# Kernel tuning notes

Measured on AMD Instinct MI355X. Metric: run time of the kernel, lower is better.

Reference implementation:

```python
import jax, jax.numpy as jnp
import numpy as np

NUM_NODES = 50000
NUM_HYPEREDGES = 20000
NNZ = 1600000
IN_DIM = 256
OUT_DIM = 128


def setup_inputs() -> dict:
    key = jax.random.key(0)
    k1, k2, k3, k4, k5 = jax.random.split(key, 5)
    x = jax.random.normal(k1, (NUM_NODES, IN_DIM), dtype=jnp.float32)
    node_idx = jax.random.randint(k2, (NNZ,), 0, NUM_NODES)
    edge_idx = jax.random.randint(k3, (NNZ,), 0, NUM_HYPEREDGES)
    hyperedge_index = jnp.stack([node_idx, edge_idx], axis=0)  # [2, nnz]
    # glorot-style init for HypergraphConv's internal Linear (bias=False)
    scale = np.sqrt(6.0 / (IN_DIM + OUT_DIM)).astype(np.float32)
    lin_weight = jax.random.uniform(k4, (IN_DIM, OUT_DIM), dtype=jnp.float32,
                                    minval=-scale, maxval=scale)
    bias = jnp.zeros((OUT_DIM,), dtype=jnp.float32)
    return {"x_node_features": x, "lin_weight": lin_weight, "bias": bias,
            "hyperedge_index": hyperedge_index}


def reference(x_node_features, lin_weight, bias, hyperedge_index):
    src = hyperedge_index[0]   # node ids   [nnz]
    edge = hyperedge_index[1]  # hyperedge ids [nnz]
    ones = jnp.ones_like(src, dtype=x_node_features.dtype)

    # X Theta
    xw = x_node_features @ lin_weight  # [N, F_out]

    # D^{-1}: node degree (hyperedge weights default to 1)
    deg_n = jax.ops.segment_sum(ones, src, num_segments=NUM_NODES)
    d_inv = jnp.where(deg_n > 0, 1.0 / deg_n, 0.0)
    # B^{-1}: hyperedge cardinality
    deg_e = jax.ops.segment_sum(ones, edge, num_segments=NUM_HYPEREDGES)
    b_inv = jnp.where(deg_e > 0, 1.0 / deg_e, 0.0)

    # node -> hyperedge: m_e = B_e^{-1} * sum_{i in e} (X Theta)_i
    m_e = jax.ops.segment_sum(xw[src], edge, num_segments=NUM_HYPEREDGES)
    m_e = m_e * b_inv[:, None]  # [E, F_out]

    # hyperedge -> node: out_i = D_i^{-1} * sum_{e ni i} m_e
    out = jax.ops.segment_sum(m_e[edge], src, num_segments=NUM_NODES)
    out = out * d_inv[:, None] + bias  # [N, F_out]

    # ReLU + mean pool over nodes
    return jnp.mean(jax.nn.relu(out), axis=0)  # [F_out]
```

## Files before the change

kernel.cpp:

```cpp
#include <hip/hip_runtime.h>

#define NUM_N 50000
#define NUM_E 20000
#define IN_DIM 256
#define OUT_DIM 128
#define NBE 1250
#define NBN 1563
#define ECAP 1536
#define NCAP 1280
#define SCAT_CHUNK 4096
#define NGEMM 782
#define XSCALE 16.0f

typedef unsigned short ushort_t;
typedef unsigned int uint_t;

__device__ __forceinline__ int clamp8(int q) { return min(max(q, -127), 127); }
__device__ __forceinline__ int lo8(uint_t u) { return (int)(signed char)(u & 0xff); }
__device__ __forceinline__ int hi8(uint_t u) { return ((int)(short)(ushort_t)u) >> 8; }

__global__ void init_kernel(int* __restrict__ gcur_e, int* __restrict__ gcur_n,
                            float* __restrict__ macc) {
    int t = blockIdx.x * 1024 + threadIdx.x;
    if (t < NBE) gcur_e[t] = t * ECAP;
    if (t < NBN) gcur_n[t] = t * NCAP;
    if (t < 128) macc[t] = 0.f;
}

__global__ __launch_bounds__(256) void gemm_scatter_kernel(
        const float* __restrict__ x, const float* __restrict__ w,
        char* __restrict__ xw, int nrows,
        const int* __restrict__ node_idx, const int* __restrict__ edge_idx, int nnz,
        int* __restrict__ gcur_e, int* __restrict__ gcur_n,
        uint_t* __restrict__ stag_e, uint_t* __restrict__ stag_n) {
    __shared__ int smem[6208];
    int tid = threadIdx.x;

    if (blockIdx.x >= NGEMM) {
        int* lh    = smem;
        int* lbase = smem + 2813;
        int bid = blockIdx.x - NGEMM;
        int nblk = gridDim.x - NGEMM;
        for (int cbase = bid * SCAT_CHUNK; cbase < nnz; cbase += nblk * SCAT_CHUNK) {
            int cend = min(cbase + SCAT_CHUNK, nnz);
            for (int i = tid; i < NBE + NBN; i += 256) lh[i] = 0;
            __syncthreads();
            for (int i = cbase + tid; i < cend; i += 256) {
                atomicAdd(&lh[edge_idx[i] >> 4], 1);
                atomicAdd(&lh[NBE + (node_idx[i] >> 5)], 1);
            }
            __syncthreads();
            for (int i = tid; i < NBE; i += 256) {
                int c = lh[i];
                lbase[i] = c ? atomicAdd(&gcur_e[i], c) : 0;
            }
            for (int i = tid; i < NBN; i += 256) {
                int c = lh[NBE + i];
                lbase[NBE + i] = c ? atomicAdd(&gcur_n[i], c) : 0;
            }
            __syncthreads();
            for (int i = tid; i < NBE + NBN; i += 256) lh[i] = 0;
            __syncthreads();
            for (int i = cbase + tid; i < cend; i += 256) {
                int v = node_idx[i];
                int e = edge_idx[i];
                uint_t pk = ((uint_t)v << 16) | (uint_t)e;
                int be = e >> 4;
                int bn = NBE + (v >> 5);
                int pe = lbase[be] + atomicAdd(&lh[be], 1);
                if (pe < (be + 1) * ECAP) stag_e[pe] = pk;
                int pn = lbase[bn] + atomicAdd(&lh[bn], 1);
                if (pn < (bn - NBE + 1) * NCAP) stag_n[pn] = pk;
            }
            __syncthreads();
        }
        return;
    }

    float* As = (float*)smem;
    float* Ws = (float*)smem + 2112;
    int block_row = blockIdx.x * 64;
    int rg = tid >> 4;
    int cg = tid & 15;
    int r0 = rg * 4, c0 = cg * 8;
    float acc[4][8] = {};
    for (int k0 = 0; k0 < IN_DIM; k0 += 32) {
#pragma unroll
        for (int rep = 0; rep < 2; ++rep) {
            int f = tid + rep * 256;
            int row = f >> 3, kq = f & 7;
            float4 v = make_float4(0.f, 0.f, 0.f, 0.f);
            int grow = block_row + row;
            if (grow < nrows) v = *(const float4*)&x[(size_t)grow * IN_DIM + k0 + kq * 4];
            As[row * 33 + kq * 4 + 0] = v.x;
            As[row * 33 + kq * 4 + 1] = v.y;
            As[row * 33 + kq * 4 + 2] = v.z;
            As[row * 33 + kq * 4 + 3] = v.w;
        }
#pragma unroll
        for (int rep = 0; rep < 4; ++rep) {
            int f = tid + rep * 256;
            int kk = f >> 5, cq = f & 31;
            float4 v = *(const float4*)&w[(size_t)(k0 + kk) * OUT_DIM + cq * 4];
            *(float4*)&Ws[kk * 128 + cq * 4] = v;
        }
        __syncthreads();
#pragma unroll
        for (int k = 0; k < 32; ++k) {
            float av[4];
#pragma unroll
            for (int i = 0; i < 4; ++i) av[i] = As[(r0 + i) * 33 + k];
            float4 b0 = *(const float4*)&Ws[k * 128 + c0];
            float4 b1 = *(const float4*)&Ws[k * 128 + c0 + 4];
            float bv[8] = {b0.x, b0.y, b0.z, b0.w, b1.x, b1.y, b1.z, b1.w};
#pragma unroll
            for (int i = 0; i < 4; ++i)
#pragma unroll
                for (int j = 0; j < 8; ++j)
                    acc[i][j] += av[i] * bv[j];
        }
        __syncthreads();
    }
#pragma unroll
    for (int i = 0; i < 4; ++i) {
        int grow = block_row + r0 + i;
        if (grow < nrows) {
            int q[8];
#pragma unroll
            for (int j = 0; j < 8; ++j) q[j] = clamp8(__float2int_rn(acc[i][j] * XSCALE));
            uint2 pk;
            pk.x = (uint_t)(q[0] & 0xff) | ((uint_t)(q[1] & 0xff) << 8) |
                   ((uint_t)(q[2] & 0xff) << 16) | ((uint_t)(q[3] & 0xff) << 24);
            pk.y = (uint_t)(q[4] & 0xff) | ((uint_t)(q[5] & 0xff) << 8) |
                   ((uint_t)(q[6] & 0xff) << 16) | ((uint_t)(q[7] & 0xff) << 24);
            *(uint2*)&xw[(size_t)grow * OUT_DIM + c0] = pk;
        }
    }
}

__global__ __launch_bounds__(256) void edge_agg_kernel(const uint_t* __restrict__ stag_e,
                                                       const int* __restrict__ gcur_e,
                                                       const ushort_t* __restrict__ xw16,
                                                       ushort_t* __restrict__ me16) {
    __shared__ int acc[16 * 128];
    __shared__ int cnt[16];
    int tid = threadIdx.x;
    int lane = tid & 63;
    int wid = tid >> 6;
    int b = blockIdx.x;
    for (int i = tid; i < 16 * 128; i += 256) acc[i] = 0;
    if (tid < 16) cnt[tid] = 0;
    __syncthreads();
    int beg = b * ECAP, end = gcur_e[b];
    int cb = beg + wid * 8;
    for (; cb + 8 <= end; cb += 32) {
        uint4 pa = *(const uint4*)&stag_e[cb];
        uint4 pb = *(const uint4*)&stag_e[cb + 4];
        uint_t u0 = xw16[(size_t)(pa.x >> 16) * 64 + lane];
        uint_t u1 = xw16[(size_t)(pa.y >> 16) * 64 + lane];
        uint_t u2 = xw16[(size_t)(pa.z >> 16) * 64 + lane];
        uint_t u3 = xw16[(size_t)(pa.w >> 16) * 64 + lane];
        uint_t u4 = xw16[(size_t)(pb.x >> 16) * 64 + lane];
        uint_t u5 = xw16[(size_t)(pb.y >> 16) * 64 + lane];
        uint_t u6 = xw16[(size_t)(pb.z >> 16) * 64 + lane];
        uint_t u7 = xw16[(size_t)(pb.w >> 16) * 64 + lane];
        int r0 = (pa.x & 15) * 128, r1 = (pa.y & 15) * 128;
        int r2 = (pa.z & 15) * 128, r3 = (pa.w & 15) * 128;
        int r4 = (pb.x & 15) * 128, r5 = (pb.y & 15) * 128;
        int r6 = (pb.z & 15) * 128, r7 = (pb.w & 15) * 128;
        atomicAdd(&acc[r0 + lane],      lo8(u0));
        atomicAdd(&acc[r0 + 64 + lane], hi8(u0));
        atomicAdd(&acc[r1 + lane],      lo8(u1));
        atomicAdd(&acc[r1 + 64 + lane], hi8(u1));
        atomicAdd(&acc[r2 + lane],      lo8(u2));
        atomicAdd(&acc[r2 + 64 + lane], hi8(u2));
        atomicAdd(&acc[r3 + lane],      lo8(u3));
        atomicAdd(&acc[r3 + 64 + lane], hi8(u3));
        atomicAdd(&acc[r4 + lane],      lo8(u4));
        atomicAdd(&acc[r4 + 64 + lane], hi8(u4));
        atomicAdd(&acc[r5 + lane],      lo8(u5));
        atomicAdd(&acc[r5 + 64 + lane], hi8(u5));
        atomicAdd(&acc[r6 + lane],      lo8(u6));
        atomicAdd(&acc[r6 + 64 + lane], hi8(u6));
        atomicAdd(&acc[r7 + lane],      lo8(u7));
        atomicAdd(&acc[r7 + 64 + lane], hi8(u7));
        if (lane == 0) {
            atomicAdd(&cnt[pa.x & 15], 1);
            atomicAdd(&cnt[pa.y & 15], 1);
            atomicAdd(&cnt[pa.z & 15], 1);
            atomicAdd(&cnt[pa.w & 15], 1);
            atomicAdd(&cnt[pb.x & 15], 1);
            atomicAdd(&cnt[pb.y & 15], 1);
            atomicAdd(&cnt[pb.z & 15], 1);
            atomicAdd(&cnt[pb.w & 15], 1);
        }
    }
    if (cb < end) {
        uint4 pa = *(const uint4*)&stag_e[cb];
        uint4 pb = *(const uint4*)&stag_e[cb + 4];
        int m = end - cb;
        bool w1 = m > 1, w2 = m > 2, w3 = m > 3, w4 = m > 4, w5 = m > 5, w6 = m > 6;
        uint_t u0 = xw16[(size_t)(pa.x >> 16) * 64 + lane];
        uint_t u1 = xw16[(size_t)(pa.y >> 16) * 64 + lane];
        uint_t u2 = xw16[(size_t)(pa.z >> 16) * 64 + lane];
        uint_t u3 = xw16[(size_t)(pa.w >> 16) * 64 + lane];
        uint_t u4 = xw16[(size_t)(pb.x >> 16) * 64 + lane];
        uint_t u5 = xw16[(size_t)(pb.y >> 16) * 64 + lane];
        uint_t u6 = xw16[(size_t)(pb.z >> 16) * 64 + lane];
        int r0 = (pa.x & 15) * 128, r1 = (pa.y & 15) * 128;
        int r2 = (pa.z & 15) * 128, r3 = (pa.w & 15) * 128;
        int r4 = (pb.x & 15) * 128, r5 = (pb.y & 15) * 128, r6 = (pb.z & 15) * 128;
        atomicAdd(&acc[r0 + lane],      lo8(u0));
        atomicAdd(&acc[r0 + 64 + lane], hi8(u0));
        atomicAdd(&acc[r1 + lane],      w1 ? lo8(u1) : 0);
        atomicAdd(&acc[r1 + 64 + lane], w1 ? hi8(u1) : 0);
        atomicAdd(&acc[r2 + lane],      w2 ? lo8(u2) : 0);
        atomicAdd(&acc[r2 + 64 + lane], w2 ? hi8(u2) : 0);
        atomicAdd(&acc[r3 + lane],      w3 ? lo8(u3) : 0);
        atomicAdd(&acc[r3 + 64 + lane], w3 ? hi8(u3) : 0);
        atomicAdd(&acc[r4 + lane],      w4 ? lo8(u4) : 0);
        atomicAdd(&acc[r4 + 64 + lane], w4 ? hi8(u4) : 0);
        atomicAdd(&acc[r5 + lane],      w5 ? lo8(u5) : 0);
        atomicAdd(&acc[r5 + 64 + lane], w5 ? hi8(u5) : 0);
        atomicAdd(&acc[r6 + lane],      w6 ? lo8(u6) : 0);
        atomicAdd(&acc[r6 + 64 + lane], w6 ? hi8(u6) : 0);
        if (lane == 0) {
            atomicAdd(&cnt[pa.x & 15], 1);
            if (w1) atomicAdd(&cnt[pa.y & 15], 1);
            if (w2) atomicAdd(&cnt[pa.z & 15], 1);
            if (w3) atomicAdd(&cnt[pa.w & 15], 1);
            if (w4) atomicAdd(&cnt[pb.x & 15], 1);
            if (w5) atomicAdd(&cnt[pb.y & 15], 1);
            if (w6) atomicAdd(&cnt[pb.z & 15], 1);
        }
    }
    __syncthreads();
    for (int r = wid; r < 16; r += 4) {
        int e = b * 16 + r;
        int c = cnt[r];
        float f = c ? 4.0f / (float)c : 0.f;
        int q0 = clamp8(__float2int_rn((float)acc[r * 128 + lane] * f));
        int q1 = clamp8(__float2int_rn((float)acc[r * 128 + 64 + lane] * f));
        me16[(size_t)e * 64 + lane] = (ushort_t)((q0 & 0xff) | ((q1 & 0xff) << 8));
    }
}

__global__ __launch_bounds__(256) void node_agg_kernel(const uint_t* __restrict__ stag_n,
                                                       const int* __restrict__ gcur_n,
                                                       const ushort_t* __restrict__ me16,
                                                       const float* __restrict__ bias,
                                                       float* __restrict__ mean_acc) {
    __shared__ int acc[32 * 128];
    __shared__ int cnt[32];
    int tid = threadIdx.x;
    int lane = tid & 63;
    int wid = tid >> 6;
    int b = blockIdx.x;
    for (int i = tid; i < 32 * 128; i += 256) acc[i] = 0;
    if (tid < 32) cnt[tid] = 0;
    __syncthreads();
    int beg = b * NCAP, end = gcur_n[b];
    int cb = beg + wid * 8;
    for (; cb + 8 <= end; cb += 32) {
        uint4 pa = *(const uint4*)&stag_n[cb];
        uint4 pb = *(const uint4*)&stag_n[cb + 4];
        uint_t u0 = me16[(size_t)(pa.x & 0xffff) * 64 + lane];
        uint_t u1 = me16[(size_t)(pa.y & 0xffff) * 64 + lane];
        uint_t u2 = me16[(size_t)(pa.z & 0xffff) * 64 + lane];
        uint_t u3 = me16[(size_t)(pa.w & 0xffff) * 64 + lane];
        uint_t u4 = me16[(size_t)(pb.x & 0xffff) * 64 + lane];
        uint_t u5 = me16[(size_t)(pb.y & 0xffff) * 64 + lane];
        uint_t u6 = me16[(size_t)(pb.z & 0xffff) * 64 + lane];
        uint_t u7 = me16[(size_t)(pb.w & 0xffff) * 64 + lane];
        int r0 = ((pa.x >> 16) & 31) * 128, r1 = ((pa.y >> 16) & 31) * 128;
        int r2 = ((pa.z >> 16) & 31) * 128, r3 = ((pa.w >> 16) & 31) * 128;
        int r4 = ((pb.x >> 16) & 31) * 128, r5 = ((pb.y >> 16) & 31) * 128;
        int r6 = ((pb.z >> 16) & 31) * 128, r7 = ((pb.w >> 16) & 31) * 128;
        atomicAdd(&acc[r0 + lane],      lo8(u0));
        atomicAdd(&acc[r0 + 64 + lane], hi8(u0));
        atomicAdd(&acc[r1 + lane],      lo8(u1));
        atomicAdd(&acc[r1 + 64 + lane], hi8(u1));
        atomicAdd(&acc[r2 + lane],      lo8(u2));
        atomicAdd(&acc[r2 + 64 + lane], hi8(u2));
        atomicAdd(&acc[r3 + lane],      lo8(u3));
        atomicAdd(&acc[r3 + 64 + lane], hi8(u3));
        atomicAdd(&acc[r4 + lane],      lo8(u4));
        atomicAdd(&acc[r4 + 64 + lane], hi8(u4));
        atomicAdd(&acc[r5 + lane],      lo8(u5));
        atomicAdd(&acc[r5 + 64 + lane], hi8(u5));
        atomicAdd(&acc[r6 + lane],      lo8(u6));
        atomicAdd(&acc[r6 + 64 + lane], hi8(u6));
        atomicAdd(&acc[r7 + lane],      lo8(u7));
        atomicAdd(&acc[r7 + 64 + lane], hi8(u7));
        if (lane == 0) {
            atomicAdd(&cnt[(pa.x >> 16) & 31], 1);
            atomicAdd(&cnt[(pa.y >> 16) & 31], 1);
            atomicAdd(&cnt[(pa.z >> 16) & 31], 1);
            atomicAdd(&cnt[(pa.w >> 16) & 31], 1);
            atomicAdd(&cnt[(pb.x >> 16) & 31], 1);
            atomicAdd(&cnt[(pb.y >> 16) & 31], 1);
            atomicAdd(&cnt[(pb.z >> 16) & 31], 1);
            atomicAdd(&cnt[(pb.w >> 16) & 31], 1);
        }
    }
    if (cb < end) {
        uint4 pa = *(const uint4*)&stag_n[cb];
        uint4 pb = *(const uint4*)&stag_n[cb + 4];
        int m = end - cb;
        bool w1 = m > 1, w2 = m > 2, w3 = m > 3, w4 = m > 4, w5 = m > 5, w6 = m > 6;
        uint_t u0 = me16[(size_t)(pa.x & 0xffff) * 64 + lane];
        uint_t u1 = me16[(size_t)(pa.y & 0xffff) * 64 + lane];
        uint_t u2 = me16[(size_t)(pa.z & 0xffff) * 64 + lane];
        uint_t u3 = me16[(size_t)(pa.w & 0xffff) * 64 + lane];
        uint_t u4 = me16[(size_t)(pb.x & 0xffff) * 64 + lane];
        uint_t u5 = me16[(size_t)(pb.y & 0xffff) * 64 + lane];
        uint_t u6 = me16[(size_t)(pb.z & 0xffff) * 64 + lane];
        int r0 = ((pa.x >> 16) & 31) * 128, r1 = ((pa.y >> 16) & 31) * 128;
        int r2 = ((pa.z >> 16) & 31) * 128, r3 = ((pa.w >> 16) & 31) * 128;
        int r4 = ((pb.x >> 16) & 31) * 128, r5 = ((pb.y >> 16) & 31) * 128;
        int r6 = ((pb.z >> 16) & 31) * 128;
        atomicAdd(&acc[r0 + lane],      lo8(u0));
        atomicAdd(&acc[r0 + 64 + lane], hi8(u0));
        atomicAdd(&acc[r1 + lane],      w1 ? lo8(u1) : 0);
        atomicAdd(&acc[r1 + 64 + lane], w1 ? hi8(u1) : 0);
        atomicAdd(&acc[r2 + lane],      w2 ? lo8(u2) : 0);
        atomicAdd(&acc[r2 + 64 + lane], w2 ? hi8(u2) : 0);
        atomicAdd(&acc[r3 + lane],      w3 ? lo8(u3) : 0);
        atomicAdd(&acc[r3 + 64 + lane], w3 ? hi8(u3) : 0);
        atomicAdd(&acc[r4 + lane],      w4 ? lo8(u4) : 0);
        atomicAdd(&acc[r4 + 64 + lane], w4 ? hi8(u4) : 0);
        atomicAdd(&acc[r5 + lane],      w5 ? lo8(u5) : 0);
        atomicAdd(&acc[r5 + 64 + lane], w5 ? hi8(u5) : 0);
        atomicAdd(&acc[r6 + lane],      w6 ? lo8(u6) : 0);
        atomicAdd(&acc[r6 + 64 + lane], w6 ? hi8(u6) : 0);
        if (lane == 0) {
            atomicAdd(&cnt[(pa.x >> 16) & 31], 1);
            if (w1) atomicAdd(&cnt[(pa.y >> 16) & 31], 1);
            if (w2) atomicAdd(&cnt[(pa.z >> 16) & 31], 1);
            if (w3) atomicAdd(&cnt[(pa.w >> 16) & 31], 1);
            if (w4) atomicAdd(&cnt[(pb.x >> 16) & 31], 1);
            if (w5) atomicAdd(&cnt[(pb.y >> 16) & 31], 1);
            if (w6) atomicAdd(&cnt[(pb.z >> 16) & 31], 1);
        }
    }
    __syncthreads();
    if (tid < 128) {
        int c = tid;
        int sw = (c & 1) ? (64 + (c >> 1)) : (c >> 1);
        float bc = bias[c];
        float s = 0.f;
        int nmax = min(32, NUM_N - b * 32);
        for (int r = 0; r < nmax; ++r) {
            int cc = cnt[r];
            float dinv = cc ? 1.0f / (64.0f * (float)cc) : 0.f;
            s += fmaxf((float)acc[r * 128 + sw] * dinv + bc, 0.f);
        }
        atomicAdd(&mean_acc[c], s);
    }
}

__global__ void finalize_kernel(const float* __restrict__ mean_acc, float* __restrict__ out) {
    int t = threadIdx.x;
    if (t < 128) out[t] = mean_acc[t] * (1.0f / (float)NUM_N);
}

extern "C" void kernel_launch(void* const* d_in, const int* in_sizes, int n_in,
                              void* d_out, int out_size, void* d_ws, size_t ws_size,
                              hipStream_t stream) {
    const float* x    = (const float*)d_in[0];
    const float* w    = (const float*)d_in[1];
    const float* bias = (const float*)d_in[2];
    const int*   hei  = (const int*)d_in[3];
    int nnz = in_sizes[3] / 2;
    const int* node_idx = hei;
    const int* edge_idx = hei + nnz;
    float* out = (float*)d_out;

    char* ws = (char*)d_ws;
    char*     xw     = ws;
    ushort_t* me16   = (ushort_t*)(ws + 6400000);
    uint_t*   stag_e = (uint_t*)(ws + 8960000);
    uint_t*   stag_n = (uint_t*)(ws + 16640032);
    int* gcur_e = (int*)(ws + 24642624);
    int* gcur_n = (int*)(ws + 24647624);
    float* macc = (float*)(ws + 24653876);

    int nscat = (nnz + SCAT_CHUNK - 1) / SCAT_CHUNK;

    init_kernel<<<2, 1024, 0, stream>>>(gcur_e, gcur_n, macc);
    gemm_scatter_kernel<<<NGEMM + nscat, 256, 0, stream>>>(
        x, w, xw, NUM_N, node_idx, edge_idx, nnz, gcur_e, gcur_n, stag_e, stag_n);

    edge_agg_kernel<<<NBE, 256, 0, stream>>>(stag_e, gcur_e, (const ushort_t*)xw, me16);
    node_agg_kernel<<<NBN, 256, 0, stream>>>(stag_n, gcur_n, me16, bias, macc);
    finalize_kernel<<<1, 128, 0, stream>>>(macc, out);
}
```

Before: 220.9 us.

## Shard global bucket cursors into eight classes to reduce atomic contention

The scatter blocks now reserve space in one of eight per-class copies of each edge and node bucket, selected by block index, instead of a single shared cursor per bucket. The aggregation kernels then loop over all eight class sub-buckets for their bucket. The aim is to cut contention on the global atomicAdd cursors during the scatter phase. In exchange the workspace grows, there are more cursors to initialise, and the reads become fragmented into eight smaller ranges with more tail handling. The smaller per-class capacities also raise the chance that a sub-bucket overflows and entries are silently dropped.

```diff
diff --git a/kernel.cpp b/kernel.cpp
--- a/kernel.cpp
+++ b/kernel.cpp
@@ -6,8 +6,9 @@
 #define OUT_DIM 128
 #define NBE 1250
 #define NBN 1563
-#define ECAP 1536
-#define NCAP 1280
+#define NCLS 8
+#define ECAPC 256
+#define NCAPC 192
 #define SCAT_CHUNK 4096
 #define NGEMM 782
 #define XSCALE 16.0f
@@ -22,8 +23,8 @@
 __global__ void init_kernel(int* __restrict__ gcur_e, int* __restrict__ gcur_n,
                             float* __restrict__ macc) {
     int t = blockIdx.x * 1024 + threadIdx.x;
-    if (t < NBE) gcur_e[t] = t * ECAP;
-    if (t < NBN) gcur_n[t] = t * NCAP;
+    if (t < NCLS * NBE) gcur_e[t] = t * ECAPC;
+    if (t < NCLS * NBN) gcur_n[t] = t * NCAPC;
     if (t < 128) macc[t] = 0.f;
 }
 
@@ -39,6 +40,7 @@
     if (blockIdx.x >= NGEMM) {
         int* lh    = smem;
         int* lbase = smem + 2813;
+        int cls = blockIdx.x & (NCLS - 1);
         int bid = blockIdx.x - NGEMM;
         int nblk = gridDim.x - NGEMM;
         for (int cbase = bid * SCAT_CHUNK; cbase < nnz; cbase += nblk * SCAT_CHUNK) {
@@ -52,11 +54,11 @@
             __syncthreads();
             for (int i = tid; i < NBE; i += 256) {
                 int c = lh[i];
-                lbase[i] = c ? atomicAdd(&gcur_e[i], c) : 0;
+                lbase[i] = c ? atomicAdd(&gcur_e[cls * NBE + i], c) : 0;
             }
             for (int i = tid; i < NBN; i += 256) {
                 int c = lh[NBE + i];
-                lbase[NBE + i] = c ? atomicAdd(&gcur_n[i], c) : 0;
+                lbase[NBE + i] = c ? atomicAdd(&gcur_n[cls * NBN + i], c) : 0;
             }
             __syncthreads();
             for (int i = tid; i < NBE + NBN; i += 256) lh[i] = 0;
@@ -66,11 +68,11 @@
                 int e = edge_idx[i];
                 uint_t pk = ((uint_t)v << 16) | (uint_t)e;
                 int be = e >> 4;
-                int bn = NBE + (v >> 5);
+                int bn = v >> 5;
                 int pe = lbase[be] + atomicAdd(&lh[be], 1);
-                if (pe < (be + 1) * ECAP) stag_e[pe] = pk;
-                int pn = lbase[bn] + atomicAdd(&lh[bn], 1);
-                if (pn < (bn - NBE + 1) * NCAP) stag_n[pn] = pk;
+                if (pe < (cls * NBE + be + 1) * ECAPC) stag_e[pe] = pk;
+                int pn = lbase[NBE + bn] + atomicAdd(&lh[NBE + bn], 1);
+                if (pn < (cls * NBN + bn + 1) * NCAPC) stag_n[pn] = pk;
             }
             __syncthreads();
         }
@@ -151,87 +153,91 @@
     for (int i = tid; i < 16 * 128; i += 256) acc[i] = 0;
     if (tid < 16) cnt[tid] = 0;
     __syncthreads();
-    int beg = b * ECAP, end = gcur_e[b];
-    int cb = beg + wid * 8;
-    for (; cb + 8 <= end; cb += 32) {
-        uint4 pa = *(const uint4*)&stag_e[cb];
-        uint4 pb = *(const uint4*)&stag_e[cb + 4];
-        uint_t u0 = xw16[(size_t)(pa.x >> 16) * 64 + lane];
-        uint_t u1 = xw16[(size_t)(pa.y >> 16) * 64 + lane];
-        uint_t u2 = xw16[(size_t)(pa.z >> 16) * 64 + lane];
-        uint_t u3 = xw16[(size_t)(pa.w >> 16) * 64 + lane];
-        uint_t u4 = xw16[(size_t)(pb.x >> 16) * 64 + lane];
-        uint_t u5 = xw16[(size_t)(pb.y >> 16) * 64 + lane];
-        uint_t u6 = xw16[(size_t)(pb.z >> 16) * 64 + lane];
-        uint_t u7 = xw16[(size_t)(pb.w >> 16) * 64 + lane];
-        int r0 = (pa.x & 15) * 128, r1 = (pa.y & 15) * 128;
-        int r2 = (pa.z & 15) * 128, r3 = (pa.w & 15) * 128;
-        int r4 = (pb.x & 15) * 128, r5 = (pb.y & 15) * 128;
-        int r6 = (pb.z & 15) * 128, r7 = (pb.w & 15) * 128;
-        atomicAdd(&acc[r0 + lane],      lo8(u0));
-        atomicAdd(&acc[r0 + 64 + lane], hi8(u0));
-        atomicAdd(&acc[r1 + lane],      lo8(u1));
-        atomicAdd(&acc[r1 + 64 + lane], hi8(u1));
-        atomicAdd(&acc[r2 + lane],      lo8(u2));
-        atomicAdd(&acc[r2 + 64 + lane], hi8(u2));
-        atomicAdd(&acc[r3 + lane],      lo8(u3));
-        atomicAdd(&acc[r3 + 64 + lane], hi8(u3));
-        atomicAdd(&acc[r4 + lane],      lo8(u4));
-        atomicAdd(&acc[r4 + 64 + lane], hi8(u4));
-        atomicAdd(&acc[r5 + lane],      lo8(u5));
-        atomicAdd(&acc[r5 + 64 + lane], hi8(u5));
-        atomicAdd(&acc[r6 + lane],      lo8(u6));
-        atomicAdd(&acc[r6 + 64 + lane], hi8(u6));
-        atomicAdd(&acc[r7 + lane],      lo8(u7));
-        atomicAdd(&acc[r7 + 64 + lane], hi8(u7));
-        if (lane == 0) {
-            atomicAdd(&cnt[pa.x & 15], 1);
-            atomicAdd(&cnt[pa.y & 15], 1);
-            atomicAdd(&cnt[pa.z & 15], 1);
-            atomicAdd(&cnt[pa.w & 15], 1);
-            atomicAdd(&cnt[pb.x & 15], 1);
-            atomicAdd(&cnt[pb.y & 15], 1);
-            atomicAdd(&cnt[pb.z & 15], 1);
-            atomicAdd(&cnt[pb.w & 15], 1);
-        }
-    }
-    if (cb < end) {
-        uint4 pa = *(const uint4*)&stag_e[cb];
-        uint4 pb = *(const uint4*)&stag_e[cb + 4];
-        int m = end - cb;
-        bool w1 = m > 1, w2 = m > 2, w3 = m > 3, w4 = m > 4, w5 = m > 5, w6 = m > 6;
-        uint_t u0 = xw16[(size_t)(pa.x >> 16) * 64 + lane];
-        uint_t u1 = xw16[(size_t)(pa.y >> 16) * 64 + lane];
-        uint_t u2 = xw16[(size_t)(pa.z >> 16) * 64 + lane];
-        uint_t u3 = xw16[(size_t)(pa.w >> 16) * 64 + lane];
-        uint_t u4 = xw16[(size_t)(pb.x >> 16) * 64 + lane];
-        uint_t u5 = xw16[(size_t)(pb.y >> 16) * 64 + lane];
-        uint_t u6 = xw16[(size_t)(pb.z >> 16) * 64 + lane];
-        int r0 = (pa.x & 15) * 128, r1 = (pa.y & 15) * 128;
-        int r2 = (pa.z & 15) * 128, r3 = (pa.w & 15) * 128;
-        int r4 = (pb.x & 15) * 128, r5 = (pb.y & 15) * 128, r6 = (pb.z & 15) * 128;
-        atomicAdd(&acc[r0 + lane],      lo8(u0));
-        atomicAdd(&acc[r0 + 64 + lane], hi8(u0));
-        atomicAdd(&acc[r1 + lane],      w1 ? lo8(u1) : 0);
-        atomicAdd(&acc[r1 + 64 + lane], w1 ? hi8(u1) : 0);
-        atomicAdd(&acc[r2 + lane],      w2 ? lo8(u2) : 0);
-        atomicAdd(&acc[r2 + 64 + lane], w2 ? hi8(u2) : 0);
-        atomicAdd(&acc[r3 + lane],      w3 ? lo8(u3) : 0);
-        atomicAdd(&acc[r3 + 64 + lane], w3 ? hi8(u3) : 0);
-        atomicAdd(&acc[r4 + lane],      w4 ? lo8(u4) : 0);
-        atomicAdd(&acc[r4 + 64 + lane], w4 ? hi8(u4) : 0);
-        atomicAdd(&acc[r5 + lane],      w5 ? lo8(u5) : 0);
-        atomicAdd(&acc[r5 + 64 + lane], w5 ? hi8(u5) : 0);
-        atomicAdd(&acc[r6 + lane],      w6 ? lo8(u6) : 0);
-        atomicAdd(&acc[r6 + 64 + lane], w6 ? hi8(u6) : 0);
-        if (lane == 0) {
-            atomicAdd(&cnt[pa.x & 15], 1);
-            if (w1) atomicAdd(&cnt[pa.y & 15], 1);
-            if (w2) atomicAdd(&cnt[pa.z & 15], 1);
-            if (w3) atomicAdd(&cnt[pa.w & 15], 1);
-            if (w4) atomicAdd(&cnt[pb.x & 15], 1);
-            if (w5) atomicAdd(&cnt[pb.y & 15], 1);
-            if (w6) atomicAdd(&cnt[pb.z & 15], 1);
+    for (int cls = 0; cls < NCLS; ++cls) {
+        int idx = cls * NBE + b;
+        int beg = idx * ECAPC;
+        int end = min(gcur_e[idx], beg + ECAPC);
+        int cb = beg + wid * 8;
+        for (; cb + 8 <= end; cb += 32) {
+            uint4 pa = *(const uint4*)&stag_e[cb];
+            uint4 pb = *(const uint4*)&stag_e[cb + 4];
+            uint_t u0 = xw16[(size_t)(pa.x >> 16) * 64 + lane];
+            uint_t u1 = xw16[(size_t)(pa.y >> 16) * 64 + lane];
+            uint_t u2 = xw16[(size_t)(pa.z >> 16) * 64 + lane];
+            uint_t u3 = xw16[(size_t)(pa.w >> 16) * 64 + lane];
+            uint_t u4 = xw16[(size_t)(pb.x >> 16) * 64 + lane];
+            uint_t u5 = xw16[(size_t)(pb.y >> 16) * 64 + lane];
+            uint_t u6 = xw16[(size_t)(pb.z >> 16) * 64 + lane];
+            uint_t u7 = xw16[(size_t)(pb.w >> 16) * 64 + lane];
+            int r0 = (pa.x & 15) * 128, r1 = (pa.y & 15) * 128;
+            int r2 = (pa.z & 15) * 128, r3 = (pa.w & 15) * 128;
+            int r4 = (pb.x & 15) * 128, r5 = (pb.y & 15) * 128;
+            int r6 = (pb.z & 15) * 128, r7 = (pb.w & 15) * 128;
+            atomicAdd(&acc[r0 + lane],      lo8(u0));
+            atomicAdd(&acc[r0 + 64 + lane], hi8(u0));
+            atomicAdd(&acc[r1 + lane],      lo8(u1));
+            atomicAdd(&acc[r1 + 64 + lane], hi8(u1));
+            atomicAdd(&acc[r2 + lane],      lo8(u2));
+            atomicAdd(&acc[r2 + 64 + lane], hi8(u2));
+            atomicAdd(&acc[r3 + lane],      lo8(u3));
+            atomicAdd(&acc[r3 + 64 + lane], hi8(u3));
+            atomicAdd(&acc[r4 + lane],      lo8(u4));
+            atomicAdd(&acc[r4 + 64 + lane], hi8(u4));
+            atomicAdd(&acc[r5 + lane],      lo8(u5));
+            atomicAdd(&acc[r5 + 64 + lane], hi8(u5));
+            atomicAdd(&acc[r6 + lane],      lo8(u6));
+            atomicAdd(&acc[r6 + 64 + lane], hi8(u6));
+            atomicAdd(&acc[r7 + lane],      lo8(u7));
+            atomicAdd(&acc[r7 + 64 + lane], hi8(u7));
+            if (lane == 0) {
+                atomicAdd(&cnt[pa.x & 15], 1);
+                atomicAdd(&cnt[pa.y & 15], 1);
+                atomicAdd(&cnt[pa.z & 15], 1);
+                atomicAdd(&cnt[pa.w & 15], 1);
+                atomicAdd(&cnt[pb.x & 15], 1);
+                atomicAdd(&cnt[pb.y & 15], 1);
+                atomicAdd(&cnt[pb.z & 15], 1);
+                atomicAdd(&cnt[pb.w & 15], 1);
+            }
+        }
+        if (cb < end) {
+            uint4 pa = *(const uint4*)&stag_e[cb];
+            uint4 pb = *(const uint4*)&stag_e[cb + 4];
+            int m = end - cb;
+            bool w1 = m > 1, w2 = m > 2, w3 = m > 3, w4 = m > 4, w5 = m > 5, w6 = m > 6;
+            uint_t u0 = xw16[(size_t)(pa.x >> 16) * 64 + lane];
+            uint_t u1 = xw16[(size_t)(pa.y >> 16) * 64 + lane];
+            uint_t u2 = xw16[(size_t)(pa.z >> 16) * 64 + lane];
+            uint_t u3 = xw16[(size_t)(pa.w >> 16) * 64 + lane];
+            uint_t u4 = xw16[(size_t)(pb.x >> 16) * 64 + lane];
+            uint_t u5 = xw16[(size_t)(pb.y >> 16) * 64 + lane];
+            uint_t u6 = xw16[(size_t)(pb.z >> 16) * 64 + lane];
+            int r0 = (pa.x & 15) * 128, r1 = (pa.y & 15) * 128;
+            int r2 = (pa.z & 15) * 128, r3 = (pa.w & 15) * 128;
+            int r4 = (pb.x & 15) * 128, r5 = (pb.y & 15) * 128, r6 = (pb.z & 15) * 128;
+            atomicAdd(&acc[r0 + lane],      lo8(u0));
+            atomicAdd(&acc[r0 + 64 + lane], hi8(u0));
+            atomicAdd(&acc[r1 + lane],      w1 ? lo8(u1) : 0);
+            atomicAdd(&acc[r1 + 64 + lane], w1 ? hi8(u1) : 0);
+            atomicAdd(&acc[r2 + lane],      w2 ? lo8(u2) : 0);
+            atomicAdd(&acc[r2 + 64 + lane], w2 ? hi8(u2) : 0);
+            atomicAdd(&acc[r3 + lane],      w3 ? lo8(u3) : 0);
+            atomicAdd(&acc[r3 + 64 + lane], w3 ? hi8(u3) : 0);
+            atomicAdd(&acc[r4 + lane],      w4 ? lo8(u4) : 0);
+            atomicAdd(&acc[r4 + 64 + lane], w4 ? hi8(u4) : 0);
+            atomicAdd(&acc[r5 + lane],      w5 ? lo8(u5) : 0);
+            atomicAdd(&acc[r5 + 64 + lane], w5 ? hi8(u5) : 0);
+            atomicAdd(&acc[r6 + lane],      w6 ? lo8(u6) : 0);
+            atomicAdd(&acc[r6 + 64 + lane], w6 ? hi8(u6) : 0);
+            if (lane == 0) {
+                atomicAdd(&cnt[pa.x & 15], 1);
+                if (w1) atomicAdd(&cnt[pa.y & 15], 1);
+                if (w2) atomicAdd(&cnt[pa.z & 15], 1);
+                if (w3) atomicAdd(&cnt[pa.w & 15], 1);
+                if (w4) atomicAdd(&cnt[pb.x & 15], 1);
+                if (w5) atomicAdd(&cnt[pb.y & 15], 1);
+                if (w6) atomicAdd(&cnt[pb.z & 15], 1);
+            }
         }
     }
     __syncthreads();
@@ -259,88 +265,92 @@
     for (int i = tid; i < 32 * 128; i += 256) acc[i] = 0;
     if (tid < 32) cnt[tid] = 0;
     __syncthreads();
-    int beg = b * NCAP, end = gcur_n[b];
-    int cb = beg + wid * 8;
-    for (; cb + 8 <= end; cb += 32) {
-        uint4 pa = *(const uint4*)&stag_n[cb];
-        uint4 pb = *(const uint4*)&stag_n[cb + 4];
-        uint_t u0 = me16[(size_t)(pa.x & 0xffff) * 64 + lane];
-        uint_t u1 = me16[(size_t)(pa.y & 0xffff) * 64 + lane];
-        uint_t u2 = me16[(size_t)(pa.z & 0xffff) * 64 + lane];
-        uint_t u3 = me16[(size_t)(pa.w & 0xffff) * 64 + lane];
-        uint_t u4 = me16[(size_t)(pb.x & 0xffff) * 64 + lane];
-        uint_t u5 = me16[(size_t)(pb.y & 0xffff) * 64 + lane];
-        uint_t u6 = me16[(size_t)(pb.z & 0xffff) * 64 + lane];
-        uint_t u7 = me16[(size_t)(pb.w & 0xffff) * 64 + lane];
-        int r0 = ((pa.x >> 16) & 31) * 128, r1 = ((pa.y >> 16) & 31) * 128;
-        int r2 = ((pa.z >> 16) & 31) * 128, r3 = ((pa.w >> 16) & 31) * 128;
-        int r4 = ((pb.x >> 16) & 31) * 128, r5 = ((pb.y >> 16) & 31) * 128;
-        int r6 = ((pb.z >> 16) & 31) * 128, r7 = ((pb.w >> 16) & 31) * 128;
-        atomicAdd(&acc[r0 + lane],      lo8(u0));
-        atomicAdd(&acc[r0 + 64 + lane], hi8(u0));
-        atomicAdd(&acc[r1 + lane],      lo8(u1));
-        atomicAdd(&acc[r1 + 64 + lane], hi8(u1));
-        atomicAdd(&acc[r2 + lane],      lo8(u2));
-        atomicAdd(&acc[r2 + 64 + lane], hi8(u2));
-        atomicAdd(&acc[r3 + lane],      lo8(u3));
-        atomicAdd(&acc[r3 + 64 + lane], hi8(u3));
-        atomicAdd(&acc[r4 + lane],      lo8(u4));
-        atomicAdd(&acc[r4 + 64 + lane], hi8(u4));
-        atomicAdd(&acc[r5 + lane],      lo8(u5));
-        atomicAdd(&acc[r5 + 64 + lane], hi8(u5));
-        atomicAdd(&acc[r6 + lane],      lo8(u6));
-        atomicAdd(&acc[r6 + 64 + lane], hi8(u6));
-        atomicAdd(&acc[r7 + lane],      lo8(u7));
-        atomicAdd(&acc[r7 + 64 + lane], hi8(u7));
-        if (lane == 0) {
-            atomicAdd(&cnt[(pa.x >> 16) & 31], 1);
-            atomicAdd(&cnt[(pa.y >> 16) & 31], 1);
-            atomicAdd(&cnt[(pa.z >> 16) & 31], 1);
-            atomicAdd(&cnt[(pa.w >> 16) & 31], 1);
-            atomicAdd(&cnt[(pb.x >> 16) & 31], 1);
-            atomicAdd(&cnt[(pb.y >> 16) & 31], 1);
-            atomicAdd(&cnt[(pb.z >> 16) & 31], 1);
-            atomicAdd(&cnt[(pb.w >> 16) & 31], 1);
-        }
-    }
-    if (cb < end) {
-        uint4 pa = *(const uint4*)&stag_n[cb];
-        uint4 pb = *(const uint4*)&stag_n[cb + 4];
-        int m = end - cb;
-        bool w1 = m > 1, w2 = m > 2, w3 = m > 3, w4 = m > 4, w5 = m > 5, w6 = m > 6;
-        uint_t u0 = me16[(size_t)(pa.x & 0xffff) * 64 + lane];
-        uint_t u1 = me16[(size_t)(pa.y & 0xffff) * 64 + lane];
-        uint_t u2 = me16[(size_t)(pa.z & 0xffff) * 64 + lane];
-        uint_t u3 = me16[(size_t)(pa.w & 0xffff) * 64 + lane];
-        uint_t u4 = me16[(size_t)(pb.x & 0xffff) * 64 + lane];
-        uint_t u5 = me16[(size_t)(pb.y & 0xffff) * 64 + lane];
-        uint_t u6 = me16[(size_t)(pb.z & 0xffff) * 64 + lane];
-        int r0 = ((pa.x >> 16) & 31) * 128, r1 = ((pa.y >> 16) & 31) * 128;
-        int r2 = ((pa.z >> 16) & 31) * 128, r3 = ((pa.w >> 16) & 31) * 128;
-        int r4 = ((pb.x >> 16) & 31) * 128, r5 = ((pb.y >> 16) & 31) * 128;
-        int r6 = ((pb.z >> 16) & 31) * 128;
-        atomicAdd(&acc[r0 + lane],      lo8(u0));
-        atomicAdd(&acc[r0 + 64 + lane], hi8(u0));
-        atomicAdd(&acc[r1 + lane],      w1 ? lo8(u1) : 0);
-        atomicAdd(&acc[r1 + 64 + lane], w1 ? hi8(u1) : 0);
-        atomicAdd(&acc[r2 + lane],      w2 ? lo8(u2) : 0);
-        atomicAdd(&acc[r2 + 64 + lane], w2 ? hi8(u2) : 0);
-        atomicAdd(&acc[r3 + lane],      w3 ? lo8(u3) : 0);
-        atomicAdd(&acc[r3 + 64 + lane], w3 ? hi8(u3) : 0);
-        atomicAdd(&acc[r4 + lane],      w4 ? lo8(u4) : 0);
-        atomicAdd(&acc[r4 + 64 + lane], w4 ? hi8(u4) : 0);
-        atomicAdd(&acc[r5 + lane],      w5 ? lo8(u5) : 0);
-        atomicAdd(&acc[r5 + 64 + lane], w5 ? hi8(u5) : 0);
-        atomicAdd(&acc[r6 + lane],      w6 ? lo8(u6) : 0);
-        atomicAdd(&acc[r6 + 64 + lane], w6 ? hi8(u6) : 0);
-        if (lane == 0) {
-            atomicAdd(&cnt[(pa.x >> 16) & 31], 1);
-            if (w1) atomicAdd(&cnt[(pa.y >> 16) & 31], 1);
-            if (w2) atomicAdd(&cnt[(pa.z >> 16) & 31], 1);
-            if (w3) atomicAdd(&cnt[(pa.w >> 16) & 31], 1);
-            if (w4) atomicAdd(&cnt[(pb.x >> 16) & 31], 1);
-            if (w5) atomicAdd(&cnt[(pb.y >> 16) & 31], 1);
-            if (w6) atomicAdd(&cnt[(pb.z >> 16) & 31], 1);
+    for (int cls = 0; cls < NCLS; ++cls) {
+        int idx = cls * NBN + b;
+        int beg = idx * NCAPC;
+        int end = min(gcur_n[idx], beg + NCAPC);
+        int cb = beg + wid * 8;
+        for (; cb + 8 <= end; cb += 32) {
+            uint4 pa = *(const uint4*)&stag_n[cb];
+            uint4 pb = *(const uint4*)&stag_n[cb + 4];
+            uint_t u0 = me16[(size_t)(pa.x & 0xffff) * 64 + lane];
+            uint_t u1 = me16[(size_t)(pa.y & 0xffff) * 64 + lane];
+            uint_t u2 = me16[(size_t)(pa.z & 0xffff) * 64 + lane];
+            uint_t u3 = me16[(size_t)(pa.w & 0xffff) * 64 + lane];
+            uint_t u4 = me16[(size_t)(pb.x & 0xffff) * 64 + lane];
+            uint_t u5 = me16[(size_t)(pb.y & 0xffff) * 64 + lane];
+            uint_t u6 = me16[(size_t)(pb.z & 0xffff) * 64 + lane];
+            uint_t u7 = me16[(size_t)(pb.w & 0xffff) * 64 + lane];
+            int r0 = ((pa.x >> 16) & 31) * 128, r1 = ((pa.y >> 16) & 31) * 128;
+            int r2 = ((pa.z >> 16) & 31) * 128, r3 = ((pa.w >> 16) & 31) * 128;
+            int r4 = ((pb.x >> 16) & 31) * 128, r5 = ((pb.y >> 16) & 31) * 128;
+            int r6 = ((pb.z >> 16) & 31) * 128, r7 = ((pb.w >> 16) & 31) * 128;
+            atomicAdd(&acc[r0 + lane],      lo8(u0));
+            atomicAdd(&acc[r0 + 64 + lane], hi8(u0));
+            atomicAdd(&acc[r1 + lane],      lo8(u1));
+            atomicAdd(&acc[r1 + 64 + lane], hi8(u1));
+            atomicAdd(&acc[r2 + lane],      lo8(u2));
+            atomicAdd(&acc[r2 + 64 + lane], hi8(u2));
+            atomicAdd(&acc[r3 + lane],      lo8(u3));
+            atomicAdd(&acc[r3 + 64 + lane], hi8(u3));
+            atomicAdd(&acc[r4 + lane],      lo8(u4));
+            atomicAdd(&acc[r4 + 64 + lane], hi8(u4));
+            atomicAdd(&acc[r5 + lane],      lo8(u5));
+            atomicAdd(&acc[r5 + 64 + lane], hi8(u5));
+            atomicAdd(&acc[r6 + lane],      lo8(u6));
+            atomicAdd(&acc[r6 + 64 + lane], hi8(u6));
+            atomicAdd(&acc[r7 + lane],      lo8(u7));
+            atomicAdd(&acc[r7 + 64 + lane], hi8(u7));
+            if (lane == 0) {
+                atomicAdd(&cnt[(pa.x >> 16) & 31], 1);
+                atomicAdd(&cnt[(pa.y >> 16) & 31], 1);
+                atomicAdd(&cnt[(pa.z >> 16) & 31], 1);
+                atomicAdd(&cnt[(pa.w >> 16) & 31], 1);
+                atomicAdd(&cnt[(pb.x >> 16) & 31], 1);
+                atomicAdd(&cnt[(pb.y >> 16) & 31], 1);
+                atomicAdd(&cnt[(pb.z >> 16) & 31], 1);
+                atomicAdd(&cnt[(pb.w >> 16) & 31], 1);
+            }
+        }
+        if (cb < end) {
+            uint4 pa = *(const uint4*)&stag_n[cb];
+            uint4 pb = *(const uint4*)&stag_n[cb + 4];
+            int m = end - cb;
+            bool w1 = m > 1, w2 = m > 2, w3 = m > 3, w4 = m > 4, w5 = m > 5, w6 = m > 6;
+            uint_t u0 = me16[(size_t)(pa.x & 0xffff) * 64 + lane];
+            uint_t u1 = me16[(size_t)(pa.y & 0xffff) * 64 + lane];
+            uint_t u2 = me16[(size_t)(pa.z & 0xffff) * 64 + lane];
+            uint_t u3 = me16[(size_t)(pa.w & 0xffff) * 64 + lane];
+            uint_t u4 = me16[(size_t)(pb.x & 0xffff) * 64 + lane];
+            uint_t u5 = me16[(size_t)(pb.y & 0xffff) * 64 + lane];
+            uint_t u6 = me16[(size_t)(pb.z & 0xffff) * 64 + lane];
+            int r0 = ((pa.x >> 16) & 31) * 128, r1 = ((pa.y >> 16) & 31) * 128;
+            int r2 = ((pa.z >> 16) & 31) * 128, r3 = ((pa.w >> 16) & 31) * 128;
+            int r4 = ((pb.x >> 16) & 31) * 128, r5 = ((pb.y >> 16) & 31) * 128;
+            int r6 = ((pb.z >> 16) & 31) * 128;
+            atomicAdd(&acc[r0 + lane],      lo8(u0));
+            atomicAdd(&acc[r0 + 64 + lane], hi8(u0));
+            atomicAdd(&acc[r1 + lane],      w1 ? lo8(u1) : 0);
+            atomicAdd(&acc[r1 + 64 + lane], w1 ? hi8(u1) : 0);
+            atomicAdd(&acc[r2 + lane],      w2 ? lo8(u2) : 0);
+            atomicAdd(&acc[r2 + 64 + lane], w2 ? hi8(u2) : 0);
+            atomicAdd(&acc[r3 + lane],      w3 ? lo8(u3) : 0);
+            atomicAdd(&acc[r3 + 64 + lane], w3 ? hi8(u3) : 0);
+            atomicAdd(&acc[r4 + lane],      w4 ? lo8(u4) : 0);
+            atomicAdd(&acc[r4 + 64 + lane], w4 ? hi8(u4) : 0);
+            atomicAdd(&acc[r5 + lane],      w5 ? lo8(u5) : 0);
+            atomicAdd(&acc[r5 + 64 + lane], w5 ? hi8(u5) : 0);
+            atomicAdd(&acc[r6 + lane],      w6 ? lo8(u6) : 0);
+            atomicAdd(&acc[r6 + 64 + lane], w6 ? hi8(u6) : 0);
+            if (lane == 0) {
+                atomicAdd(&cnt[(pa.x >> 16) & 31], 1);
+                if (w1) atomicAdd(&cnt[(pa.y >> 16) & 31], 1);
+                if (w2) atomicAdd(&cnt[(pa.z >> 16) & 31], 1);
+                if (w3) atomicAdd(&cnt[(pa.w >> 16) & 31], 1);
+                if (w4) atomicAdd(&cnt[(pb.x >> 16) & 31], 1);
+                if (w5) atomicAdd(&cnt[(pb.y >> 16) & 31], 1);
+                if (w6) atomicAdd(&cnt[(pb.z >> 16) & 31], 1);
+            }
         }
     }
     __syncthreads();
@@ -380,14 +390,14 @@
     char*     xw     = ws;
     ushort_t* me16   = (ushort_t*)(ws + 6400000);
     uint_t*   stag_e = (uint_t*)(ws + 8960000);
-    uint_t*   stag_n = (uint_t*)(ws + 16640032);
-    int* gcur_e = (int*)(ws + 24642624);
-    int* gcur_n = (int*)(ws + 24647624);
-    float* macc = (float*)(ws + 24653876);
+    uint_t*   stag_n = (uint_t*)(ws + 19200032);
+    int* gcur_e = (int*)(ws + 28803136);
+    int* gcur_n = (int*)(ws + 28843136);
+    float* macc = (float*)(ws + 28893152);
 
     int nscat = (nnz + SCAT_CHUNK - 1) / SCAT_CHUNK;
 
-    init_kernel<<<2, 1024, 0, stream>>>(gcur_e, gcur_n, macc);
+    init_kernel<<<13, 1024, 0, stream>>>(gcur_e, gcur_n, macc);
     gemm_scatter_kernel<<<NGEMM + nscat, 256, 0, stream>>>(
         x, w, xw, NUM_N, node_idx, edge_idx, nnz, gcur_e, gcur_n, stag_e, stag_n);
 
```

Result: faster. 211.0 us (-4.5%).
